# Performance work log

Measured on AMD Instinct MI355X. Metric: run time of the kernel, lower is better.

Reference implementation:

```python
import jax, jax.numpy as jnp
import numpy as np

B, T, C, H = 4, 2048, 1024, 16
D = C // H  # head_dim = 64


def setup_inputs() -> dict:
    key = jax.random.key(0)
    k1, k2, k3, k4 = jax.random.split(key, 4)
    x = jax.random.normal(k1, (B, T, C), dtype=jnp.float32)
    # realistic padding: each sequence has length in [T//2, T]
    lengths = jax.random.randint(k4, (B,), T // 2, T + 1)
    padding_mask = jnp.arange(T)[None, :] < lengths[:, None]  # True = keep
    # weights stored [in, out] (equivalent to torch Linear weight transposed)
    w_qkv = jax.random.normal(k2, (C, 3 * C), dtype=jnp.float32) * (C ** -0.5)
    w_out = jax.random.normal(k3, (C, C), dtype=jnp.float32) * (C ** -0.5)
    b_out = jnp.zeros((C,), dtype=jnp.float32)
    return {"x": x, "padding_mask": padding_mask, "w_qkv": w_qkv, "w_out": w_out, "b_out": b_out}


def reference(x, padding_mask, w_qkv, w_out, b_out):
    scale = D ** -0.5
    qkv = x @ w_qkv  # [B,T,3C]
    q, k, v = jnp.split(qkv, 3, axis=-1)

    def split_heads(t):
        return t.reshape(B, T, H, D).transpose(0, 2, 1, 3)  # [B,H,T,D]

    q, k, v = split_heads(q), split_heads(k), split_heads(v)
    attn = jnp.einsum("bhqd,bhkd->bhqk", q, k) * scale  # [B,H,T,T]
    mask = padding_mask[:, None, None, :]  # [B,1,1,T]
    attn = jnp.where(mask, attn, jnp.finfo(attn.dtype).min)
    attn = jax.nn.softmax(attn, axis=-1)
    # dropout is identity in eval mode
    out = jnp.einsum("bhqk,bhkd->bhqd", attn, v)  # [B,H,T,D]
    out = out.transpose(0, 2, 1, 3).reshape(B, T, C)
    return out @ w_out + b_out
```

## Files before the change

### kernel.cpp

```cpp
#include <hip/hip_runtime.h>
#include <hip/hip_bf16.h>

#define Bb 4
#define Tt 2048
#define Cc 1024
#define Hh 16

typedef unsigned short u16;
typedef __attribute__((ext_vector_type(8))) __bf16 bf16x8;
typedef __attribute__((ext_vector_type(4))) float  f32x4;

__device__ __forceinline__ u16 f2bf_hw(float f) {
    __bf16 h = (__bf16)f;
    return *(u16*)&h;
}

__device__ __forceinline__ unsigned cvt_pk_bf16(float a, float b) {
    unsigned r;
    asm("v_cvt_pk_bf16_f32 %0, %1, %2" : "=v"(r) : "v"(a), "v"(b));
    return r;
}

__device__ __forceinline__ float fexp2(float x) {
#if __has_builtin(__builtin_amdgcn_exp2f)
    return __builtin_amdgcn_exp2f(x);
#else
    return __expf(x * 0.6931471805599453f);
#endif
}

__device__ __forceinline__ void gld_lds16(const void* g, void* l) {
    __builtin_amdgcn_global_load_lds(
        (__attribute__((address_space(1))) void*)(g),
        (__attribute__((address_space(3))) void*)(l),
        16, 0, 0);
}

__device__ __forceinline__ f32x4 mfma16(bf16x8 a, bf16x8 b, f32x4 c) {
    return __builtin_amdgcn_mfma_f32_16x16x32_bf16(a, b, c, 0, 0, 0);
}

__global__ void cast_f32_bf16(const float* __restrict__ in, u16* __restrict__ out, int n4) {
    int i = blockIdx.x * 256 + threadIdx.x;
    if (i < n4) {
        float4 v = ((const float4*)in)[i];
        uint2 o;
        o.x = cvt_pk_bf16(v.x, v.y);
        o.y = cvt_pk_bf16(v.z, v.w);
        ((uint2*)out)[i] = o;
    }
}

__global__ void castT_f32_bf16(const float* __restrict__ in, u16* __restrict__ out,
                               int K, int N, int scaleN, float sv) {
    __shared__ float Ls[64][65];
    const int n0 = blockIdx.x * 64, k0 = blockIdx.y * 64;
    const int t = threadIdx.x;
    #pragma unroll
    for (int s = 0; s < 4; ++s) {
        int idx = t + 256 * s;
        int r   = idx >> 4;
        int c4  = (idx & 15) * 4;
        float4 v = *(const float4*)&in[(size_t)(k0 + r) * N + n0 + c4];
        Ls[r][c4 + 0] = v.x; Ls[r][c4 + 1] = v.y;
        Ls[r][c4 + 2] = v.z; Ls[r][c4 + 3] = v.w;
    }
    __syncthreads();
    #pragma unroll
    for (int s = 0; s < 2; ++s) {
        int idx = t + 256 * s;
        int n   = idx >> 3;
        int kc  = (idx & 7) * 8;
        const float sc = (n0 + n < scaleN) ? sv : 1.0f;
        alignas(16) u16 tmp[8];
        #pragma unroll
        for (int i = 0; i < 8; ++i) tmp[i] = f2bf_hw(Ls[kc + i][n] * sc);
        *(uint4*)&out[(size_t)(n0 + n) * K + k0 + kc] = *(const uint4*)tmp;
    }
}

__global__ __launch_bounds__(256, 3) void gemm_bt_bf16(
    const u16* __restrict__ A, const u16* __restrict__ Bt,
    const float* __restrict__ bias,
    u16* __restrict__ outB, float* __restrict__ outF,
    int M, int N, int K)
{
    __shared__ u16 As[128 * 64];
    __shared__ u16 Bs[128 * 64];
    const int t = threadIdx.x;
    const int w = t >> 6, lane = t & 63;
    const int quad = lane >> 4, l16 = lane & 15;
    const int wm = w >> 1, wn = w & 1;
    const int m0 = blockIdx.y * 128, n0 = blockIdx.x * 128;

    const int l8r   = lane >> 3;
    const int g_log = (lane & 7) ^ l8r;
    const u16* sAp[4]; const u16* sBp[4];
    #pragma unroll
    for (int u = 0; u < 4; ++u) {
        const int gi = w * 4 + u;
        sAp[u] = A  + (size_t)(m0 + gi * 8 + l8r) * K + g_log * 8;
        sBp[u] = Bt + (size_t)(n0 + gi * 8 + l8r) * K + g_log * 8;
    }
    const int dst0 = w * 2048 + lane * 8;

    int aoff[4][2], boff[4][2];
    #pragma unroll
    for (int i = 0; i < 4; ++i) {
        const int rA = 64 * wm + 16 * i + l16;
        const int rB = 64 * wn + 16 * i + l16;
        #pragma unroll
        for (int kk = 0; kk < 2; ++kk) {
            aoff[i][kk] = rA * 64 + (((4 * kk + quad) ^ (rA & 7)) * 8);
            boff[i][kk] = rB * 64 + (((4 * kk + quad) ^ (rB & 7)) * 8);
        }
    }

    f32x4 acc[4][4] = {};

    for (int k0 = 0; k0 < K; k0 += 64) {
        __syncthreads();
        #pragma unroll
        for (int u = 0; u < 4; ++u) {
            gld_lds16(sAp[u] + k0, (void*)(As + dst0 + u * 512));
            gld_lds16(sBp[u] + k0, (void*)(Bs + dst0 + u * 512));
        }
        asm volatile("s_waitcnt vmcnt(0)" ::: "memory");
        __syncthreads();

        #pragma unroll
        for (int kk = 0; kk < 2; ++kk) {
            bf16x8 af[4], bfr[4];
            #pragma unroll
            for (int i = 0; i < 4; ++i) af[i]  = *(const bf16x8*)&As[aoff[i][kk]];
            #pragma unroll
            for (int j = 0; j < 4; ++j) bfr[j] = *(const bf16x8*)&Bs[boff[j][kk]];
            #pragma unroll
            for (int i = 0; i < 4; ++i)
                #pragma unroll
                for (int j = 0; j < 4; ++j)
                    acc[i][j] = mfma16(af[i], bfr[j], acc[i][j]);
        }
    }

    const int rbase = m0 + 64 * wm + quad * 4;
    const int cbase = n0 + 64 * wn + l16;
    if (outF) {
        float bv[4];
        #pragma unroll
        for (int j = 0; j < 4; ++j) bv[j] = bias[cbase + 16 * j];
        #pragma unroll
        for (int i = 0; i < 4; ++i)
            #pragma unroll
            for (int r = 0; r < 4; ++r) {
                size_t ro = (size_t)(rbase + 16 * i + r) * N;
                #pragma unroll
                for (int j = 0; j < 4; ++j)
                    outF[ro + cbase + 16 * j] = acc[i][j][r] + bv[j];
            }
    } else {
        #pragma unroll
        for (int i = 0; i < 4; ++i)
            #pragma unroll
            for (int r = 0; r < 4; ++r) {
                size_t ro = (size_t)(rbase + 16 * i + r) * N;
                #pragma unroll
                for (int j = 0; j < 4; ++j)
                    outB[ro + cbase + 16 * j] = f2bf_hw(acc[i][j][r]);
            }
    }
}

__global__ __launch_bounds__(256, 3) void gemm_qkv_bt(
    const u16* __restrict__ A, const u16* __restrict__ Bt,
    u16* __restrict__ outQ, u16* __restrict__ kx, u16* __restrict__ vx)
{
    const int K = Cc;
    __shared__ u16 As[128 * 64];
    __shared__ u16 Bs[128 * 64];
    const int t = threadIdx.x;
    const int w = t >> 6, lane = t & 63;
    const int quad = lane >> 4, l16 = lane & 15;
    const int wm = w >> 1, wn = w & 1;
    const int m0 = blockIdx.y * 128, n0 = blockIdx.x * 128;

    const int l8r   = lane >> 3;
    const int g_log = (lane & 7) ^ l8r;
    const u16* sAp[4]; const u16* sBp[4];
    #pragma unroll
    for (int u = 0; u < 4; ++u) {
        const int gi = w * 4 + u;
        sAp[u] = A  + (size_t)(m0 + gi * 8 + l8r) * K + g_log * 8;
        sBp[u] = Bt + (size_t)(n0 + gi * 8 + l8r) * K + g_log * 8;
    }
    const int dst0 = w * 2048 + lane * 8;

    int aoff[4][2], boff[4][2];
    #pragma unroll
    for (int i = 0; i < 4; ++i) {
        const int rA = 64 * wm + 16 * i + l16;
        const int rB = 64 * wn + 16 * i + l16;
        #pragma unroll
        for (int kk = 0; kk < 2; ++kk) {
            aoff[i][kk] = rA * 64 + (((4 * kk + quad) ^ (rA & 7)) * 8);
            boff[i][kk] = rB * 64 + (((4 * kk + quad) ^ (rB & 7)) * 8);
        }
    }

    f32x4 acc[4][4] = {};

    for (int k0 = 0; k0 < K; k0 += 64) {
        __syncthreads();
        #pragma unroll
        for (int u = 0; u < 4; ++u) {
            gld_lds16(sAp[u] + k0, (void*)(As + dst0 + u * 512));
            gld_lds16(sBp[u] + k0, (void*)(Bs + dst0 + u * 512));
        }
        asm volatile("s_waitcnt vmcnt(0)" ::: "memory");
        __syncthreads();

        #pragma unroll
        for (int kk = 0; kk < 2; ++kk) {
            bf16x8 af[4], bfr[4];
            #pragma unroll
            for (int i = 0; i < 4; ++i) af[i]  = *(const bf16x8*)&As[aoff[i][kk]];
            #pragma unroll
            for (int j = 0; j < 4; ++j) bfr[j] = *(const bf16x8*)&Bs[boff[j][kk]];
            #pragma unroll
            for (int i = 0; i < 4; ++i)
                #pragma unroll
                for (int j = 0; j < 4; ++j)
                    acc[i][j] = mfma16(af[i], bfr[j], acc[i][j]);
        }
    }

    const int rbase = m0 + 64 * wm + quad * 4;
    const int cbase = n0 + 64 * wn + l16;
    const int region = n0 >> 10;

    if (region == 0) {
        #pragma unroll
        for (int i = 0; i < 4; ++i)
            #pragma unroll
            for (int r = 0; r < 4; ++r) {
                size_t ro = (size_t)(rbase + 16 * i + r) * Cc;
                #pragma unroll
                for (int j = 0; j < 4; ++j)
                    outQ[ro + cbase + 16 * j] = f2bf_hw(acc[i][j][r]);
            }
    } else if (region == 1) {
        int colK[4];
        #pragma unroll
        for (int j = 0; j < 4; ++j) {
            const int c = (cbase - 1024) + 16 * j;
            const int h = c >> 6, d = c & 63;
            colK[j] = h * 131072 + (d >> 5) * 512 + ((d >> 3) & 3) * 128 + (d & 7);
        }
        #pragma unroll
        for (int i = 0; i < 4; ++i)
            #pragma unroll
            for (int r = 0; r < 4; ++r) {
                const int row = rbase + 16 * i + r;
                const int b = row >> 11, key = row & 2047;
                const int ch = key >> 6, keyr = key & 63;
                const int rowK = b * 2097152 + ch * 4096 + (keyr >> 4) * 1024 + (keyr & 15) * 8;
                #pragma unroll
                for (int j = 0; j < 4; ++j)
                    kx[rowK + colK[j]] = f2bf_hw(acc[i][j][r]);
            }
    } else {
        int colV[4];
        #pragma unroll
        for (int j = 0; j < 4; ++j) {
            const int c = (cbase - 2048) + 16 * j;
            const int h = c >> 6, d = c & 63;
            colV[j] = h * 131072 + (d >> 4) * 1024 + (d & 15) * 8;
        }
        #pragma unroll
        for (int i = 0; i < 4; ++i)
            #pragma unroll
            for (int r = 0; r < 4; ++r) {
                const int row = rbase + 16 * i + r;
                const int b = row >> 11, key = row & 2047;
                const int ch = key >> 6, keyr = key & 63;
                const int rowV = b * 2097152 + ch * 4096 + (keyr >> 5) * 512
                               + ((keyr >> 3) & 3) * 128 + (keyr & 7);
                #pragma unroll
                for (int j = 0; j < 4; ++j)
                    vx[rowV + colV[j]] = f2bf_hw(acc[i][j][r]);
            }
    }
}

__global__ __launch_bounds__(256, 2) void attn_mfma4(
    const u16* __restrict__ qb, const u16* __restrict__ kx, const u16* __restrict__ vx,
    const int* __restrict__ mask, u16* __restrict__ outO)
{
    __shared__ u16 KVs[8192];
    __shared__ u16 Pss[4][4][16 * 68];

    const int t = threadIdx.x;
    const int w = t >> 6, lane = t & 63;
    const int quad = lane >> 4, l16 = lane & 15;
    const int bh = blockIdx.x, qblk = blockIdx.y, b = bh >> 4, h = bh & 15;

    int sum = 0;
    {
        const int4* mp = (const int4*)(mask + b * Tt) + lane * 8;
        #pragma unroll
        for (int i = 0; i < 8; ++i) { int4 m4 = mp[i]; sum += m4.x + m4.y + m4.z + m4.w; }
        #pragma unroll
        for (int off = 1; off < 64; off <<= 1) sum += __shfl_xor(sum, off);
    }
    const int L = sum;

    const int q0 = qblk * 256 + w * 64;
    bf16x8 qf[4][2];
    #pragma unroll
    for (int qq = 0; qq < 4; ++qq) {
        const u16* qp = qb + (size_t)(b * Tt + q0 + 16 * qq + l16) * Cc + h * 64 + quad * 8;
        qf[qq][0] = *(const bf16x8*)(qp);
        qf[qq][1] = *(const bf16x8*)(qp + 32);
    }

    f32x4 oacc[4][4] = {};
    f32x4 lacc[4]    = {};
    const __bf16 onebf = (__bf16)1.0f;
    const bf16x8 ones  = {onebf, onebf, onebf, onebf, onebf, onebf, onebf, onebf};

    const int nfull = L >> 6;
    const int nch   = (L + 63) >> 6;
    const size_t cb0 = (size_t)bh * 32 * 4096;

    {
        uint4 k0a = *(const uint4*)&kx[cb0 + t * 8];
        uint4 k0b = *(const uint4*)&kx[cb0 + 2048 + t * 8];
        uint4 v0a = *(const uint4*)&vx[cb0 + t * 8];
        uint4 v0b = *(const uint4*)&vx[cb0 + 2048 + t * 8];
        *(uint4*)&KVs[t * 8]        = k0a;
        *(uint4*)&KVs[2048 + t * 8] = k0b;
        *(uint4*)&KVs[4096 + t * 8] = v0a;
        *(uint4*)&KVs[6144 + t * 8] = v0b;
    }
    __syncthreads();

    for (int ch = 0; ch < nch; ++ch) {
        const int cc = (ch + 1 < nch) ? ch + 1 : ch;
        const size_t nb = cb0 + (size_t)cc * 4096;
        uint4 nk0 = *(const uint4*)&kx[nb + t * 8];
        uint4 nk1 = *(const uint4*)&kx[nb + 2048 + t * 8];
        uint4 nv0 = *(const uint4*)&vx[nb + t * 8];
        uint4 nv1 = *(const uint4*)&vx[nb + 2048 + t * 8];

        const u16* Kb = KVs;
        const u16* Vb = KVs + 4096;

        bf16x8 kf[4][2];
        #pragma unroll
        for (int jt = 0; jt < 4; ++jt)
            #pragma unroll
            for (int ks = 0; ks < 2; ++ks)
                kf[jt][ks] = *(const bf16x8*)&Kb[(jt * 2 + ks) * 512 + lane * 8];

        bf16x8 vf[4][2];
        #pragma unroll
        for (int dt = 0; dt < 4; ++dt)
            #pragma unroll
            for (int ks = 0; ks < 2; ++ks)
                vf[dt][ks] = *(const bf16x8*)&Vb[(dt * 2 + ks) * 512 + lane * 8];

        #pragma unroll
        for (int qq = 0; qq < 4; ++qq) {
            u16* Pw = Pss[w][qq];
            f32x4 st[4];
            __builtin_amdgcn_s_setprio(1);
            #pragma unroll
            for (int jt = 0; jt < 4; ++jt) {
                f32x4 z = {0.f, 0.f, 0.f, 0.f};
                z = mfma16(kf[jt][0], qf[qq][0], z);
                st[jt] = mfma16(kf[jt][1], qf[qq][1], z);
            }
            __builtin_amdgcn_s_setprio(0);
            uint2 pk[4];
            if (ch < nfull) {
                #pragma unroll
                for (int jt = 0; jt < 4; ++jt) {
                    pk[jt].x = cvt_pk_bf16(fexp2(st[jt][0]), fexp2(st[jt][1]));
                    pk[jt].y = cvt_pk_bf16(fexp2(st[jt][2]), fexp2(st[jt][3]));
                }
            } else {
                const int kc = ch * 64;
                #pragma unroll
                for (int jt = 0; jt < 4; ++jt) {
                    const int kb = kc + 16 * jt + quad * 4;
                    float e[4];
                    #pragma unroll
                    for (int r = 0; r < 4; ++r)
                        e[r] = (kb + r < L) ? fexp2(st[jt][r]) : 0.f;
                    pk[jt].x = cvt_pk_bf16(e[0], e[1]);
                    pk[jt].y = cvt_pk_bf16(e[2], e[3]);
                }
            }
            #pragma unroll
            for (int jt = 0; jt < 4; ++jt)
                *(uint2*)&Pw[l16 * 68 + 16 * jt + quad * 4] = pk[jt];

            __builtin_amdgcn_s_setprio(1);
            #pragma unroll
            for (int ks = 0; ks < 2; ++ks) {
                const u16* pr = &Pw[l16 * 68 + 32 * ks + quad * 8];
                uint2 pa = *(const uint2*)pr;
                uint2 pb = *(const uint2*)(pr + 4);
                uint4 comb = {pa.x, pa.y, pb.x, pb.y};
                bf16x8 pf = *(const bf16x8*)&comb;
                #pragma unroll
                for (int dt = 0; dt < 4; ++dt)
                    oacc[qq][dt] = mfma16(pf, vf[dt][ks], oacc[qq][dt]);
                lacc[qq] = mfma16(pf, ones, lacc[qq]);
            }
            __builtin_amdgcn_s_setprio(0);
        }

        __syncthreads();
        *(uint4*)&KVs[t * 8]        = nk0;
        *(uint4*)&KVs[2048 + t * 8] = nk1;
        *(uint4*)&KVs[4096 + t * 8] = nv0;
        *(uint4*)&KVs[6144 + t * 8] = nv1;
        __syncthreads();
    }

    #pragma unroll
    for (int qq = 0; qq < 4; ++qq)
        #pragma unroll
        for (int r = 0; r < 4; ++r) {
            const float inv = 1.f / lacc[qq][r];
            const size_t ro = (size_t)(b * Tt + q0 + 16 * qq + quad * 4 + r) * Cc + h * 64 + l16;
            #pragma unroll
            for (int dt = 0; dt < 4; ++dt)
                outO[ro + 16 * dt] = f2bf_hw(oacc[qq][dt][r] * inv);
        }
}

extern "C" void kernel_launch(void* const* d_in, const int* in_sizes, int n_in,
                              void* d_out, int out_size, void* d_ws, size_t ws_size,
                              hipStream_t stream) {
    const float* x     = (const float*)d_in[0];
    const int*   mask  = (const int*)  d_in[1];
    const float* w_qkv = (const float*)d_in[2];
    const float* w_out = (const float*)d_in[3];
    const float* b_out = (const float*)d_in[4];
    float*       outp  = (float*)d_out;

    const int M = Bb * Tt;
    char* ws = (char*)d_ws;
    u16* xb     = (u16*)(ws);
    u16* wqkvT  = (u16*)(ws + (16u << 20));
    u16* woutT  = (u16*)(ws + (22u << 20));
    u16* qbuf   = (u16*)(ws + (24u << 20));
    u16* kx     = (u16*)(ws + (40u << 20));
    u16* vx     = (u16*)(ws + (56u << 20));
    u16* attnO  = (u16*)(ws);

    const float c2 = 0.18033688011112042f;

    cast_f32_bf16<<<(M * Cc / 4 + 255) / 256, 256, 0, stream>>>(x, xb, M * Cc / 4);
    castT_f32_bf16<<<dim3(3 * Cc / 64, Cc / 64), 256, 0, stream>>>(w_qkv, wqkvT, Cc, 3 * Cc, Cc, c2);
    castT_f32_bf16<<<dim3(Cc / 64, Cc / 64), 256, 0, stream>>>(w_out, woutT, Cc, Cc, 0, 1.0f);

    gemm_qkv_bt<<<dim3(3 * Cc / 128, M / 128), 256, 0, stream>>>(
        xb, wqkvT, qbuf, kx, vx);

    attn_mfma4<<<dim3(Bb * Hh, Tt / 256), 256, 0, stream>>>(qbuf, kx, vx, mask, attnO);

    gemm_bt_bf16<<<dim3(Cc / 128, M / 128), 256, 0, stream>>>(
        attnO, woutT, b_out, nullptr, outp, M, Cc, Cc);
}
```

Before: 253.4 us.

## Merge cast kernels into one launch and batch attention score phases

The three fp32-to-bf16 cast kernels are merged into one kernel that routes blocks by ID to the x cast or one of the two weight transposes, saving two launches. In the attention inner loop, the per-query-group sequence of QK MFMA, exp, P store and PV MFMA is split into three phases over all four query groups. This gives the scheduler more independent MFMA work to hide exp and LDS latency. The cost is more live registers for the 16 score accumulators, which could lower occupancy or cause spills.

```diff
diff --git a/kernel.cpp b/kernel.cpp
--- a/kernel.cpp
+++ b/kernel.cpp
@@ -40,21 +40,10 @@
     return __builtin_amdgcn_mfma_f32_16x16x32_bf16(a, b, c, 0, 0, 0);
 }
 
-__global__ void cast_f32_bf16(const float* __restrict__ in, u16* __restrict__ out, int n4) {
-    int i = blockIdx.x * 256 + threadIdx.x;
-    if (i < n4) {
-        float4 v = ((const float4*)in)[i];
-        uint2 o;
-        o.x = cvt_pk_bf16(v.x, v.y);
-        o.y = cvt_pk_bf16(v.z, v.w);
-        ((uint2*)out)[i] = o;
-    }
-}
-
-__global__ void castT_f32_bf16(const float* __restrict__ in, u16* __restrict__ out,
-                               int K, int N, int scaleN, float sv) {
-    __shared__ float Ls[64][65];
-    const int n0 = blockIdx.x * 64, k0 = blockIdx.y * 64;
+__device__ void castT_body(const float* __restrict__ in, u16* __restrict__ out,
+                           int K, int N, int scaleN, float sv,
+                           int bx, int by, float Ls[64][65]) {
+    const int n0 = bx * 64, k0 = by * 64;
     const int t = threadIdx.x;
     #pragma unroll
     for (int s = 0; s < 4; ++s) {
@@ -76,6 +65,28 @@
         #pragma unroll
         for (int i = 0; i < 8; ++i) tmp[i] = f2bf_hw(Ls[kc + i][n] * sc);
         *(uint4*)&out[(size_t)(n0 + n) * K + k0 + kc] = *(const uint4*)tmp;
+    }
+}
+
+__global__ void prep_cast(const float* __restrict__ x, u16* __restrict__ xb,
+                          const float* __restrict__ w_qkv, u16* __restrict__ wqkvT,
+                          const float* __restrict__ w_out, u16* __restrict__ woutT,
+                          float c2) {
+    __shared__ float Ls[64][65];
+    const int id = blockIdx.x;
+    if (id < 8192) {
+        const int i = id * 256 + threadIdx.x;
+        float4 v = ((const float4*)x)[i];
+        uint2 o;
+        o.x = cvt_pk_bf16(v.x, v.y);
+        o.y = cvt_pk_bf16(v.z, v.w);
+        ((uint2*)xb)[i] = o;
+    } else if (id < 8192 + 768) {
+        const int r = id - 8192;
+        castT_body(w_qkv, wqkvT, Cc, 3 * Cc, Cc, c2, r % 48, r / 48, Ls);
+    } else {
+        const int r = id - 8960;
+        castT_body(w_out, woutT, Cc, Cc, 0, 1.0f, r % 16, r / 16, Ls);
     }
 }
 
@@ -369,46 +380,52 @@
             for (int ks = 0; ks < 2; ++ks)
                 vf[dt][ks] = *(const bf16x8*)&Vb[(dt * 2 + ks) * 512 + lane * 8];
 
-        #pragma unroll
-        for (int qq = 0; qq < 4; ++qq) {
-            u16* Pw = Pss[w][qq];
-            f32x4 st[4];
-            __builtin_amdgcn_s_setprio(1);
+        f32x4 st[4][4];
+        __builtin_amdgcn_s_setprio(1);
+        #pragma unroll
+        for (int qq = 0; qq < 4; ++qq)
             #pragma unroll
             for (int jt = 0; jt < 4; ++jt) {
                 f32x4 z = {0.f, 0.f, 0.f, 0.f};
                 z = mfma16(kf[jt][0], qf[qq][0], z);
-                st[jt] = mfma16(kf[jt][1], qf[qq][1], z);
-            }
-            __builtin_amdgcn_s_setprio(0);
-            uint2 pk[4];
-            if (ch < nfull) {
+                st[qq][jt] = mfma16(kf[jt][1], qf[qq][1], z);
+            }
+        __builtin_amdgcn_s_setprio(0);
+
+        if (ch < nfull) {
+            #pragma unroll
+            for (int qq = 0; qq < 4; ++qq)
                 #pragma unroll
                 for (int jt = 0; jt < 4; ++jt) {
-                    pk[jt].x = cvt_pk_bf16(fexp2(st[jt][0]), fexp2(st[jt][1]));
-                    pk[jt].y = cvt_pk_bf16(fexp2(st[jt][2]), fexp2(st[jt][3]));
+                    uint2 pk;
+                    pk.x = cvt_pk_bf16(fexp2(st[qq][jt][0]), fexp2(st[qq][jt][1]));
+                    pk.y = cvt_pk_bf16(fexp2(st[qq][jt][2]), fexp2(st[qq][jt][3]));
+                    *(uint2*)&Pss[w][qq][l16 * 68 + 16 * jt + quad * 4] = pk;
                 }
-            } else {
-                const int kc = ch * 64;
+        } else {
+            const int kc = ch * 64;
+            #pragma unroll
+            for (int qq = 0; qq < 4; ++qq)
                 #pragma unroll
                 for (int jt = 0; jt < 4; ++jt) {
                     const int kb = kc + 16 * jt + quad * 4;
                     float e[4];
                     #pragma unroll
                     for (int r = 0; r < 4; ++r)
-                        e[r] = (kb + r < L) ? fexp2(st[jt][r]) : 0.f;
-                    pk[jt].x = cvt_pk_bf16(e[0], e[1]);
-                    pk[jt].y = cvt_pk_bf16(e[2], e[3]);
+                        e[r] = (kb + r < L) ? fexp2(st[qq][jt][r]) : 0.f;
+                    uint2 pk;
+                    pk.x = cvt_pk_bf16(e[0], e[1]);
+                    pk.y = cvt_pk_bf16(e[2], e[3]);
+                    *(uint2*)&Pss[w][qq][l16 * 68 + 16 * jt + quad * 4] = pk;
                 }
-            }
-            #pragma unroll
-            for (int jt = 0; jt < 4; ++jt)
-                *(uint2*)&Pw[l16 * 68 + 16 * jt + quad * 4] = pk[jt];
-
-            __builtin_amdgcn_s_setprio(1);
+        }
+
+        __builtin_amdgcn_s_setprio(1);
+        #pragma unroll
+        for (int qq = 0; qq < 4; ++qq) {
             #pragma unroll
             for (int ks = 0; ks < 2; ++ks) {
-                const u16* pr = &Pw[l16 * 68 + 32 * ks + quad * 8];
+                const u16* pr = &Pss[w][qq][l16 * 68 + 32 * ks + quad * 8];
                 uint2 pa = *(const uint2*)pr;
                 uint2 pb = *(const uint2*)(pr + 4);
                 uint4 comb = {pa.x, pa.y, pb.x, pb.y};
@@ -418,8 +435,8 @@
                     oacc[qq][dt] = mfma16(pf, vf[dt][ks], oacc[qq][dt]);
                 lacc[qq] = mfma16(pf, ones, lacc[qq]);
             }
-            __builtin_amdgcn_s_setprio(0);
-        }
+        }
+        __builtin_amdgcn_s_setprio(0);
 
         __syncthreads();
         *(uint4*)&KVs[t * 8]        = nk0;
@@ -463,9 +480,7 @@
 
     const float c2 = 0.18033688011112042f;
 
-    cast_f32_bf16<<<(M * Cc / 4 + 255) / 256, 256, 0, stream>>>(x, xb, M * Cc / 4);
-    castT_f32_bf16<<<dim3(3 * Cc / 64, Cc / 64), 256, 0, stream>>>(w_qkv, wqkvT, Cc, 3 * Cc, Cc, c2);
-    castT_f32_bf16<<<dim3(Cc / 64, Cc / 64), 256, 0, stream>>>(w_out, woutT, Cc, Cc, 0, 1.0f);
+    prep_cast<<<9216, 256, 0, stream>>>(x, xb, w_qkv, wqkvT, w_out, woutT, c2);
 
     gemm_qkv_bt<<<dim3(3 * Cc / 128, M / 128), 256, 0, stream>>>(
         xb, wqkvT, qbuf, kx, vx);
```

After: 295.0 us. +16.4%, slower.
